# Performance work log

Measured on AMD Instinct MI355X. Metric: run time of the kernel, lower is better.

## Reference

```python
import jax, jax.numpy as jnp
import numpy as np

B, F, P, H, D = 2, 128, 256, 8, 64
DIM = H * D  # dim = num_heads * head_dim


def setup_inputs() -> dict:
    key = jax.random.key(0)
    ks = jax.random.split(key, 4)
    s = 0.02  # init scale for weights
    return {
        "x": jax.random.normal(ks[0], (B, F, P, DIM), jnp.float32),
        # frame QKV: projects dim -> (qkv, heads, dim_head)
        "W_f": (jax.random.normal(ks[1], (3, H, D, DIM), jnp.float32) * s),
        "b_f": jnp.zeros((3, H, D), jnp.float32),
        # point QKV: mixes (heads_in, dim_head_in) -> (qkv, heads_out, dim_head_out)
        "W_p": (jax.random.normal(ks[2], (3, H, D, H, D), jnp.float32) * s),
        "b_p": jnp.zeros((3, H, D), jnp.float32),
        # out projection: (heads, dim_head) -> dim
        "W_o": (jax.random.normal(ks[3], (H, D, DIM), jnp.float32) * s),
        "b_o": jnp.zeros((DIM,), jnp.float32),
    }


def reference(x, W_f, b_f, W_p, b_p, W_o, b_o):
    # ---- frame attention (attend across frames, per point) ----
    # qkv: [3, b, point, frame, heads, dim_head]
    qkv = jnp.einsum('bfpd,qhed->qbpfhe', x, W_f) + b_f[:, None, None, None, :, :]
    q, k, v = qkv[0], qkv[1], qkv[2]
    # scores: [b, point, frame_q, frame_k, heads]  (NOTE: source applies no 1/sqrt(d) scaling)
    scores = jnp.einsum('bpfhe,bpghe->bpfgh', q, k)
    w = jax.nn.softmax(scores, axis=3)  # softmax over frame_key
    fa = jnp.einsum('bpfgh,bpghe->bfphe', w, v)  # [b, frame, point, heads, dim_head]

    # ---- point attention (attend across points, per frame) ----
    # qkv2: [3, b, frame, point, heads, dim_head]
    qkv2 = jnp.einsum('bfpij,qheij->qbfphe', fa, W_p) + b_p[:, None, None, None, :, :]
    q2, k2, v2 = qkv2[0], qkv2[1], qkv2[2]
    # scores2: [b, frame, point_q, point_k, heads] (no scaling, per source)
    scores2 = jnp.einsum('bfphe,bfqhe->bfpqh', q2, k2)
    w2 = jax.nn.softmax(scores2, axis=3)  # softmax over point_key
    pa = jnp.einsum('bfpqh,bfqhe->bfphe', w2, v2)  # [b, frame, point, heads, dim_head]

    # ---- output projection ----
    return jnp.einsum('bfphe,hed->bfpd', pa, W_o) + b_o
```

## Files before the change

kernel.cpp:

```cpp
#include <hip/hip_runtime.h>
#include <hip/hip_bf16.h>
#include <stdint.h>

typedef __bf16 bf16;
typedef __attribute__((ext_vector_type(8))) __bf16 bf16x8;
typedef __attribute__((ext_vector_type(4))) float f32x4;

#define B_ 2
#define F_ 128
#define P_ 256
#define H_ 8
#define D_ 64
#define DIM_ 512
#define NROWS (B_*F_*P_)

__device__ __forceinline__ void load_lds16(const void* g, void* l) {
  __builtin_amdgcn_global_load_lds(
      (__attribute__((address_space(1))) void*)(uintptr_t)g,
      (__attribute__((address_space(3))) void*)(uint32_t)(uintptr_t)l,
      16, 0, 0);
}

__global__ void cvt_f32_bf16(const float* __restrict__ src, bf16* __restrict__ dst, int n)
{
  int i = (blockIdx.x * 256 + threadIdx.x) * 8;
  if (i < n) {
    float4 a = *(const float4*)(src + i);
    float4 b = *(const float4*)(src + i + 4);
    bf16x8 o;
    o[0] = (bf16)a.x; o[1] = (bf16)a.y; o[2] = (bf16)a.z; o[3] = (bf16)a.w;
    o[4] = (bf16)b.x; o[5] = (bf16)b.y; o[6] = (bf16)b.z; o[7] = (bf16)b.w;
    *(bf16x8*)(dst + i) = o;
  }
}

__global__ void transpose_wo(const float* __restrict__ src, bf16* __restrict__ dst)
{
  int idx = blockIdx.x * 256 + threadIdx.x;
  int d = idx & 511, he = idx >> 9;
  dst[(size_t)d * 512 + he] = (bf16)src[(size_t)he * 512 + d];
}

#define BM 128
#define BN 128
#define BK 32

template <typename OutT>
__global__ __launch_bounds__(256, 2)
void gemm_bt_bias(const bf16* __restrict__ A, const bf16* __restrict__ Bt,
                  const float* __restrict__ bias, OutT* __restrict__ C,
                  int N, int K)
{
  __shared__ __align__(16) bf16 As[BM * BK];
  __shared__ __align__(16) bf16 Bs[BN * BK];

  const int t    = threadIdx.x;
  const int lane = t & 63;
  const int wave = t >> 6;
  const int wm   = wave & 1;
  const int wn   = wave >> 1;
  const int l16  = lane & 15;
  const int qd   = lane >> 4;

  const int mBase = blockIdx.y * BM;
  const int nBase = blockIdx.x * BN;

  f32x4 acc[4][4] = {};

  for (int k0 = 0; k0 < K; k0 += BK) {
    __syncthreads();
#pragma unroll
    for (int r = 0; r < 2; ++r) {
      int c = r * 256 + t;
      int row = c >> 2;
      int col = (c & 3) << 3;
      load_lds16(A  + (size_t)(mBase + row) * K + k0 + col, As + c * 8);
      load_lds16(Bt + (size_t)(nBase + row) * K + k0 + col, Bs + c * 8);
    }
    __syncthreads();

    bf16x8 a[4], b[4];
#pragma unroll
    for (int i = 0; i < 4; ++i)
      a[i] = *(const bf16x8*)(As + (wm * 64 + i * 16 + l16) * BK + qd * 8);
#pragma unroll
    for (int j = 0; j < 4; ++j)
      b[j] = *(const bf16x8*)(Bs + (wn * 64 + j * 16 + l16) * BK + qd * 8);
#pragma unroll
    for (int i = 0; i < 4; ++i)
#pragma unroll
      for (int j = 0; j < 4; ++j)
        acc[i][j] = __builtin_amdgcn_mfma_f32_16x16x32_bf16(a[i], b[j], acc[i][j], 0, 0, 0);
  }

#pragma unroll
  for (int j = 0; j < 4; ++j) {
    int coln = nBase + wn * 64 + j * 16 + l16;
    float bv = bias[coln];
#pragma unroll
    for (int i = 0; i < 4; ++i) {
      int rowm = mBase + wm * 64 + i * 16 + qd * 4;
#pragma unroll
      for (int r = 0; r < 4; ++r)
        C[(size_t)(rowm + r) * N + coln] = (OutT)(acc[i][j][r] + bv);
    }
  }
}

template <int NKB, int MODE>
__global__ __launch_bounds__(256)
void attn_kernel(const bf16* __restrict__ qkv, bf16* __restrict__ outp)
{
  __shared__ __align__(16) bf16 lds[(2 + NKB) * 8192];
  bf16* Qs = lds;
  bf16* Ks = lds + 8192;
  bf16* Vt = lds + (1 + NKB) * 8192;
  bf16* Pm = lds;

  const int t    = threadIdx.x;
  const int lane = t & 63;
  const int wave = t >> 6;
  const int l16  = lane & 15;
  const int qd   = lane >> 4;

  const int bid = blockIdx.x;
  int h, q0, rowbase, rstride;
  if (MODE == 0) {
    h = bid & 7;
    int p = (bid >> 3) & (P_ - 1);
    int b = bid >> 11;
    rowbase = b * F_ * P_ + p; rstride = P_; q0 = 0;
  } else {
    int qb = bid & 1;
    h = (bid >> 1) & 7;
    int f = (bid >> 4) & (F_ - 1);
    int b = bid >> 11;
    rowbase = (b * F_ + f) * P_; rstride = 1; q0 = qb * 128;
  }

#pragma unroll
  for (int r = 0; r < 4; ++r) {
    int c = r * 256 + t;
    int i = c >> 3, e = (c & 7) << 3;
    load_lds16(qkv + (size_t)(rowbase + (q0 + i) * rstride) * 1536 + h * 64 + e, Qs + c * 8);
  }
#pragma unroll
  for (int r = 0; r < 4 * NKB; ++r) {
    int c = r * 256 + t;
    int i = c >> 3, e = (c & 7) << 3;
    load_lds16(qkv + (size_t)(rowbase + i * rstride) * 1536 + 512 + h * 64 + e, Ks + c * 8);
  }
  __syncthreads();

  const int m0 = wave * 32;
  f32x4 acc[2][NKB * 8] = {};

  bf16x8 afr[2][2];
#pragma unroll
  for (int tm = 0; tm < 2; ++tm)
#pragma unroll
    for (int ks = 0; ks < 2; ++ks)
      afr[tm][ks] = *(const bf16x8*)(Qs + (m0 + tm * 16 + l16) * 64 + ks * 32 + qd * 8);

#pragma unroll
  for (int tn = 0; tn < NKB * 8; ++tn) {
    bf16x8 b0 = *(const bf16x8*)(Ks + (tn * 16 + l16) * 64 + qd * 8);
    bf16x8 b1 = *(const bf16x8*)(Ks + (tn * 16 + l16) * 64 + 32 + qd * 8);
#pragma unroll
    for (int tm = 0; tm < 2; ++tm) {
      acc[tm][tn] = __builtin_amdgcn_mfma_f32_16x16x32_bf16(afr[tm][0], b0, acc[tm][tn], 0, 0, 0);
      acc[tm][tn] = __builtin_amdgcn_mfma_f32_16x16x32_bf16(afr[tm][1], b1, acc[tm][tn], 0, 0, 0);
    }
  }

#pragma unroll
  for (int tm = 0; tm < 2; ++tm) {
#pragma unroll
    for (int r = 0; r < 4; ++r) {
      float m = -3.0e38f;
#pragma unroll
      for (int tn = 0; tn < NKB * 8; ++tn) m = fmaxf(m, acc[tm][tn][r]);
#pragma unroll
      for (int off = 1; off < 16; off <<= 1) m = fmaxf(m, __shfl_xor(m, off));
      float s = 0.0f;
#pragma unroll
      for (int tn = 0; tn < NKB * 8; ++tn) {
        float e0 = __expf(acc[tm][tn][r] - m);
        acc[tm][tn][r] = e0;
        s += e0;
      }
#pragma unroll
      for (int off = 1; off < 16; off <<= 1) s += __shfl_xor(s, off);
      float inv = 1.0f / s;
#pragma unroll
      for (int tn = 0; tn < NKB * 8; ++tn) acc[tm][tn][r] *= inv;
    }
  }

  f32x4 facc[2][4] = {};
#pragma unroll
  for (int kb = 0; kb < NKB; ++kb) {
    __syncthreads();
#pragma unroll
    for (int tm = 0; tm < 2; ++tm)
#pragma unroll
      for (int tj = 0; tj < 8; ++tj)
#pragma unroll
        for (int r = 0; r < 4; ++r)
          Pm[(m0 + tm * 16 + qd * 4 + r) * 128 + tj * 16 + l16] = (bf16)acc[tm][kb * 8 + tj][r];
    {
      int iloc = t >> 1;
      int eh = (t & 1) * 32;
      const bf16* src = qkv + (size_t)(rowbase + (kb * 128 + iloc) * rstride) * 1536 + 1024 + h * 64 + eh;
#pragma unroll
      for (int jj = 0; jj < 4; ++jj) {
        bf16x8 v8 = *(const bf16x8*)(src + jj * 8);
#pragma unroll
        for (int j = 0; j < 8; ++j) Vt[(eh + jj * 8 + j) * 128 + iloc] = v8[j];
      }
    }
    __syncthreads();
#pragma unroll
    for (int ks = 0; ks < 4; ++ks) {
      bf16x8 pfr[2];
#pragma unroll
      for (int tm = 0; tm < 2; ++tm)
        pfr[tm] = *(const bf16x8*)(Pm + (m0 + tm * 16 + l16) * 128 + ks * 32 + qd * 8);
#pragma unroll
      for (int tn = 0; tn < 4; ++tn) {
        bf16x8 bv = *(const bf16x8*)(Vt + (tn * 16 + l16) * 128 + ks * 32 + qd * 8);
#pragma unroll
        for (int tm = 0; tm < 2; ++tm)
          facc[tm][tn] = __builtin_amdgcn_mfma_f32_16x16x32_bf16(pfr[tm], bv, facc[tm][tn], 0, 0, 0);
      }
    }
  }

#pragma unroll
  for (int tm = 0; tm < 2; ++tm)
#pragma unroll
    for (int tn = 0; tn < 4; ++tn)
#pragma unroll
      for (int r = 0; r < 4; ++r) {
        int iq = q0 + m0 + tm * 16 + qd * 4 + r;
        outp[(size_t)(rowbase + iq * rstride) * 512 + h * 64 + tn * 16 + l16] = (bf16)facc[tm][tn][r];
      }
}

extern "C" void kernel_launch(void* const* d_in, const int* in_sizes, int n_in,
                              void* d_out, int out_size, void* d_ws, size_t ws_size,
                              hipStream_t stream)
{
  (void)in_sizes; (void)n_in; (void)out_size; (void)ws_size;
  const float* x   = (const float*)d_in[0];
  const float* Wf  = (const float*)d_in[1];
  const float* bfb = (const float*)d_in[2];
  const float* Wp  = (const float*)d_in[3];
  const float* bpb = (const float*)d_in[4];
  const float* Wo  = (const float*)d_in[5];
  const float* bob = (const float*)d_in[6];
  float* out = (float*)d_out;

  char* ws = (char*)d_ws;
  bf16* qkv = (bf16*)ws;
  bf16* fa  = (bf16*)(ws + (size_t)NROWS * 1536 * 2);
  bf16* xb  = fa;
  char* wbase = ws + (size_t)NROWS * 1536 * 2 + (size_t)NROWS * 512 * 2;
  bf16* wfb = (bf16*)wbase;
  bf16* wpb = (bf16*)(wbase + 1536 * 512 * 2);
  bf16* wot = (bf16*)(wbase + 2 * 1536 * 512 * 2);

  cvt_f32_bf16<<<(NROWS * 512) / (256 * 8), 256, 0, stream>>>(x, xb, NROWS * 512);
  cvt_f32_bf16<<<(1536 * 512) / (256 * 8), 256, 0, stream>>>(Wf, wfb, 1536 * 512);
  cvt_f32_bf16<<<(1536 * 512) / (256 * 8), 256, 0, stream>>>(Wp, wpb, 1536 * 512);
  transpose_wo<<<1024, 256, 0, stream>>>(Wo, wot);

  gemm_bt_bias<bf16><<<dim3(12, 512), 256, 0, stream>>>(xb, wfb, bfb, qkv, 1536, 512);
  attn_kernel<1, 0><<<4096, 256, 0, stream>>>(qkv, fa);
  gemm_bt_bias<bf16><<<dim3(12, 512), 256, 0, stream>>>(fa, wpb, bpb, qkv, 1536, 512);
  attn_kernel<2, 1><<<4096, 256, 0, stream>>>(qkv, fa);
  gemm_bt_bias<float><<<dim3(4, 512), 256, 0, stream>>>(fa, wot, bob, out, 512, 512);
}
```

Before: 823.1 us.

## Swizzle GEMM LDS tiles and restructure attention with transposed scores and padded LDS

```diff
diff --git a/kernel.cpp b/kernel.cpp
--- a/kernel.cpp
+++ b/kernel.cpp
@@ -4,6 +4,7 @@
 
 typedef __bf16 bf16;
 typedef __attribute__((ext_vector_type(8))) __bf16 bf16x8;
+typedef __attribute__((ext_vector_type(4))) __bf16 bf16x4;
 typedef __attribute__((ext_vector_type(4))) float f32x4;
 
 #define B_ 2
@@ -73,7 +74,7 @@
     for (int r = 0; r < 2; ++r) {
       int c = r * 256 + t;
       int row = c >> 2;
-      int col = (c & 3) << 3;
+      int col = (((c & 3) ^ (row & 3)) << 3);
       load_lds16(A  + (size_t)(mBase + row) * K + k0 + col, As + c * 8);
       load_lds16(Bt + (size_t)(nBase + row) * K + k0 + col, Bs + c * 8);
     }
@@ -81,11 +82,15 @@
 
     bf16x8 a[4], b[4];
 #pragma unroll
-    for (int i = 0; i < 4; ++i)
-      a[i] = *(const bf16x8*)(As + (wm * 64 + i * 16 + l16) * BK + qd * 8);
-#pragma unroll
-    for (int j = 0; j < 4; ++j)
-      b[j] = *(const bf16x8*)(Bs + (wn * 64 + j * 16 + l16) * BK + qd * 8);
+    for (int i = 0; i < 4; ++i) {
+      int row = wm * 64 + i * 16 + l16;
+      a[i] = *(const bf16x8*)(As + row * BK + ((qd ^ (row & 3)) << 3));
+    }
+#pragma unroll
+    for (int j = 0; j < 4; ++j) {
+      int row = wn * 64 + j * 16 + l16;
+      b[j] = *(const bf16x8*)(Bs + row * BK + ((qd ^ (row & 3)) << 3));
+    }
 #pragma unroll
     for (int i = 0; i < 4; ++i)
 #pragma unroll
@@ -107,15 +112,12 @@
   }
 }
 
-template <int NKB, int MODE>
-__global__ __launch_bounds__(256)
-void attn_kernel(const bf16* __restrict__ qkv, bf16* __restrict__ outp)
-{
-  __shared__ __align__(16) bf16 lds[(2 + NKB) * 8192];
-  bf16* Qs = lds;
-  bf16* Ks = lds + 8192;
-  bf16* Vt = lds + (1 + NKB) * 8192;
-  bf16* Pm = lds;
+template <int NKT, int MODE, int VS>
+__global__ __launch_bounds__(256, 2)
+void attn2(const bf16* __restrict__ qkv, bf16* __restrict__ outp)
+{
+  __shared__ __align__(16) bf16 Vt[64 * VS];
+  __shared__ __align__(16) bf16 Pq[128 * 136];
 
   const int t    = threadIdx.x;
   const int lane = t & 63;
@@ -139,112 +141,110 @@
   }
 
 #pragma unroll
-  for (int r = 0; r < 4; ++r) {
-    int c = r * 256 + t;
-    int i = c >> 3, e = (c & 7) << 3;
-    load_lds16(qkv + (size_t)(rowbase + (q0 + i) * rstride) * 1536 + h * 64 + e, Qs + c * 8);
-  }
-#pragma unroll
-  for (int r = 0; r < 4 * NKB; ++r) {
-    int c = r * 256 + t;
-    int i = c >> 3, e = (c & 7) << 3;
-    load_lds16(qkv + (size_t)(rowbase + i * rstride) * 1536 + 512 + h * 64 + e, Ks + c * 8);
-  }
-  __syncthreads();
-
-  const int m0 = wave * 32;
-  f32x4 acc[2][NKB * 8] = {};
-
-  bf16x8 afr[2][2];
-#pragma unroll
-  for (int tm = 0; tm < 2; ++tm)
+  for (int p = 0; p < NKT / 8; ++p) {
+    int key = p * 128 + (t >> 1);
+    int eh  = (t & 1) * 32;
+    const bf16* src = qkv + (size_t)(rowbase + key * rstride) * 1536 + 1024 + h * 64 + eh;
+    bf16x8 v[4];
+#pragma unroll
+    for (int jj = 0; jj < 4; ++jj) v[jj] = *(const bf16x8*)(src + jj * 8);
+#pragma unroll
+    for (int jj = 0; jj < 4; ++jj)
+#pragma unroll
+      for (int j = 0; j < 8; ++j)
+        Vt[(eh + jj * 8 + j) * VS + key] = v[jj][j];
+  }
+
+  const int qloc = wave * 32;
+  bf16x8 qf[2][2];
+#pragma unroll
+  for (int qt = 0; qt < 2; ++qt)
 #pragma unroll
     for (int ks = 0; ks < 2; ++ks)
-      afr[tm][ks] = *(const bf16x8*)(Qs + (m0 + tm * 16 + l16) * 64 + ks * 32 + qd * 8);
-
-#pragma unroll
-  for (int tn = 0; tn < NKB * 8; ++tn) {
-    bf16x8 b0 = *(const bf16x8*)(Ks + (tn * 16 + l16) * 64 + qd * 8);
-    bf16x8 b1 = *(const bf16x8*)(Ks + (tn * 16 + l16) * 64 + 32 + qd * 8);
-#pragma unroll
-    for (int tm = 0; tm < 2; ++tm) {
-      acc[tm][tn] = __builtin_amdgcn_mfma_f32_16x16x32_bf16(afr[tm][0], b0, acc[tm][tn], 0, 0, 0);
-      acc[tm][tn] = __builtin_amdgcn_mfma_f32_16x16x32_bf16(afr[tm][1], b1, acc[tm][tn], 0, 0, 0);
-    }
-  }
-
-#pragma unroll
-  for (int tm = 0; tm < 2; ++tm) {
-#pragma unroll
-    for (int r = 0; r < 4; ++r) {
-      float m = -3.0e38f;
-#pragma unroll
-      for (int tn = 0; tn < NKB * 8; ++tn) m = fmaxf(m, acc[tm][tn][r]);
-#pragma unroll
-      for (int off = 1; off < 16; off <<= 1) m = fmaxf(m, __shfl_xor(m, off));
-      float s = 0.0f;
-#pragma unroll
-      for (int tn = 0; tn < NKB * 8; ++tn) {
-        float e0 = __expf(acc[tm][tn][r] - m);
-        acc[tm][tn][r] = e0;
+      qf[qt][ks] = *(const bf16x8*)(qkv +
+          (size_t)(rowbase + (q0 + qloc + qt * 16 + l16) * rstride) * 1536 +
+          h * 64 + ks * 32 + qd * 8);
+
+  f32x4 sacc[NKT][2] = {};
+#pragma unroll
+  for (int tn = 0; tn < NKT; ++tn) {
+    const bf16* krow = qkv + (size_t)(rowbase + (tn * 16 + l16) * rstride) * 1536 + 512 + h * 64;
+    bf16x8 kf0 = *(const bf16x8*)(krow + qd * 8);
+    bf16x8 kf1 = *(const bf16x8*)(krow + 32 + qd * 8);
+#pragma unroll
+    for (int qt = 0; qt < 2; ++qt) {
+      sacc[tn][qt] = __builtin_amdgcn_mfma_f32_16x16x32_bf16(kf0, qf[qt][0], sacc[tn][qt], 0, 0, 0);
+      sacc[tn][qt] = __builtin_amdgcn_mfma_f32_16x16x32_bf16(kf1, qf[qt][1], sacc[tn][qt], 0, 0, 0);
+    }
+  }
+
+#pragma unroll
+  for (int qt = 0; qt < 2; ++qt) {
+    float m = -3.0e38f;
+#pragma unroll
+    for (int tn = 0; tn < NKT; ++tn)
+#pragma unroll
+      for (int r = 0; r < 4; ++r) m = fmaxf(m, sacc[tn][qt][r]);
+    m = fmaxf(m, __shfl_xor(m, 16));
+    m = fmaxf(m, __shfl_xor(m, 32));
+    float s = 0.0f;
+#pragma unroll
+    for (int tn = 0; tn < NKT; ++tn)
+#pragma unroll
+      for (int r = 0; r < 4; ++r) {
+        float e0 = __expf(sacc[tn][qt][r] - m);
+        sacc[tn][qt][r] = e0;
         s += e0;
       }
-#pragma unroll
-      for (int off = 1; off < 16; off <<= 1) s += __shfl_xor(s, off);
-      float inv = 1.0f / s;
-#pragma unroll
-      for (int tn = 0; tn < NKB * 8; ++tn) acc[tm][tn][r] *= inv;
-    }
-  }
-
-  f32x4 facc[2][4] = {};
-#pragma unroll
-  for (int kb = 0; kb < NKB; ++kb) {
-    __syncthreads();
-#pragma unroll
-    for (int tm = 0; tm < 2; ++tm)
-#pragma unroll
-      for (int tj = 0; tj < 8; ++tj)
-#pragma unroll
-        for (int r = 0; r < 4; ++r)
-          Pm[(m0 + tm * 16 + qd * 4 + r) * 128 + tj * 16 + l16] = (bf16)acc[tm][kb * 8 + tj][r];
-    {
-      int iloc = t >> 1;
-      int eh = (t & 1) * 32;
-      const bf16* src = qkv + (size_t)(rowbase + (kb * 128 + iloc) * rstride) * 1536 + 1024 + h * 64 + eh;
-#pragma unroll
-      for (int jj = 0; jj < 4; ++jj) {
-        bf16x8 v8 = *(const bf16x8*)(src + jj * 8);
-#pragma unroll
-        for (int j = 0; j < 8; ++j) Vt[(eh + jj * 8 + j) * 128 + iloc] = v8[j];
+    s += __shfl_xor(s, 16);
+    s += __shfl_xor(s, 32);
+    float inv = 1.0f / s;
+#pragma unroll
+    for (int tn = 0; tn < NKT; ++tn)
+#pragma unroll
+      for (int r = 0; r < 4; ++r) sacc[tn][qt][r] *= inv;
+  }
+
+  f32x4 oacc[4][2] = {};
+#pragma unroll
+  for (int hf = 0; hf < NKT / 8; ++hf) {
+#pragma unroll
+    for (int qt = 0; qt < 2; ++qt)
+#pragma unroll
+      for (int tl = 0; tl < 8; ++tl) {
+        int tn = hf * 8 + tl;
+        bf16x4 pk;
+#pragma unroll
+        for (int r = 0; r < 4; ++r) pk[r] = (bf16)sacc[tn][qt][r];
+        *(bf16x4*)(Pq + (qloc + qt * 16 + l16) * 136 + tl * 16 + qd * 4) = pk;
       }
-    }
-    __syncthreads();
+    if (hf == 0) __syncthreads();
 #pragma unroll
     for (int ks = 0; ks < 4; ++ks) {
-      bf16x8 pfr[2];
-#pragma unroll
-      for (int tm = 0; tm < 2; ++tm)
-        pfr[tm] = *(const bf16x8*)(Pm + (m0 + tm * 16 + l16) * 128 + ks * 32 + qd * 8);
-#pragma unroll
-      for (int tn = 0; tn < 4; ++tn) {
-        bf16x8 bv = *(const bf16x8*)(Vt + (tn * 16 + l16) * 128 + ks * 32 + qd * 8);
-#pragma unroll
-        for (int tm = 0; tm < 2; ++tm)
-          facc[tm][tn] = __builtin_amdgcn_mfma_f32_16x16x32_bf16(pfr[tm], bv, facc[tm][tn], 0, 0, 0);
+      bf16x8 pf[2];
+#pragma unroll
+      for (int qt = 0; qt < 2; ++qt)
+        pf[qt] = *(const bf16x8*)(Pq + (qloc + qt * 16 + l16) * 136 + ks * 32 + qd * 8);
+#pragma unroll
+      for (int te = 0; te < 4; ++te) {
+        bf16x8 vf = *(const bf16x8*)(Vt + (te * 16 + l16) * VS + hf * 128 + ks * 32 + qd * 8);
+#pragma unroll
+        for (int qt = 0; qt < 2; ++qt)
+          oacc[te][qt] = __builtin_amdgcn_mfma_f32_16x16x32_bf16(vf, pf[qt], oacc[te][qt], 0, 0, 0);
       }
     }
   }
 
 #pragma unroll
-  for (int tm = 0; tm < 2; ++tm)
-#pragma unroll
-    for (int tn = 0; tn < 4; ++tn)
-#pragma unroll
-      for (int r = 0; r < 4; ++r) {
-        int iq = q0 + m0 + tm * 16 + qd * 4 + r;
-        outp[(size_t)(rowbase + iq * rstride) * 512 + h * 64 + tn * 16 + l16] = (bf16)facc[tm][tn][r];
-      }
+  for (int te = 0; te < 4; ++te)
+#pragma unroll
+    for (int qt = 0; qt < 2; ++qt) {
+      int q = q0 + qloc + qt * 16 + l16;
+      bf16x4 pk;
+#pragma unroll
+      for (int r = 0; r < 4; ++r) pk[r] = (bf16)oacc[te][qt][r];
+      *(bf16x4*)(outp + (size_t)(rowbase + q * rstride) * 512 + h * 64 + te * 16 + qd * 4) = pk;
+    }
 }
 
 extern "C" void kernel_launch(void* const* d_in, const int* in_sizes, int n_in,
@@ -276,8 +276,8 @@
   transpose_wo<<<1024, 256, 0, stream>>>(Wo, wot);
 
   gemm_bt_bias<bf16><<<dim3(12, 512), 256, 0, stream>>>(xb, wfb, bfb, qkv, 1536, 512);
-  attn_kernel<1, 0><<<4096, 256, 0, stream>>>(qkv, fa);
+  attn2<8, 0, 136><<<4096, 256, 0, stream>>>(qkv, fa);
   gemm_bt_bias<bf16><<<dim3(12, 512), 256, 0, stream>>>(fa, wpb, bpb, qkv, 1536, 512);
-  attn_kernel<2, 1><<<4096, 256, 0, stream>>>(qkv, fa);
+  attn2<16, 1, 272><<<4096, 256, 0, stream>>>(qkv, fa);
   gemm_bt_bias<float><<<dim3(4, 512), 256, 0, stream>>>(fa, wot, bob, out, 512, 512);
 }
```

Measured after the change: 772.4 us. 6.2% less time.
